# Kernel tuning notes

Hardware: AMD Instinct MI355X
Metric: run time of the kernel (lower is better)

## Reference

```python
import jax, jax.numpy as jnp
import numpy as np

NEG = -1e30


def setup_inputs() -> dict:
    key = jax.random.key(0)
    k1, k2, k3, k4 = jax.random.split(key, 4)
    B, L, T, M = 64, 256, 1600, 80
    probs = jax.random.uniform(k1, (B, L, T), dtype=jnp.float32)
    melspec = jax.random.normal(k2, (B, M, T), dtype=jnp.float32)
    text_lengths = jax.random.randint(k3, (B,), 1, L + 1)   # values in [1, L]
    mel_lengths = jax.random.randint(k4, (B,), 1, T + 1)    # values in [1, T]
    return {"probs": probs, "melspec": melspec,
            "text_lengths": text_lengths, "mel_lengths": mel_lengths}


def reference(probs, melspec, text_lengths, mel_lengths):
    B, L, _ = probs.shape
    T = melspec.shape[2]
    log_prob_matrix = jnp.log(probs + 1e-30)            # [B, L, T]
    lp_t = jnp.moveaxis(log_prob_matrix, 2, 0)          # [T, B, L]

    # t = 0: only (l=0, t=0) is alive
    init = jnp.full((B, L), NEG, dtype=log_prob_matrix.dtype)
    init = init.at[:, 0].set(lp_t[0, :, 0])

    def step(prev, lp):
        # stay at label l, or advance from label l-1 (monotonic alignment)
        shifted = jnp.concatenate(
            [jnp.full((B, 1), NEG, dtype=prev.dtype), prev[:, :-1]], axis=1)
        new = jnp.logaddexp(prev, shifted) + lp
        return new, new

    _, ys = jax.lax.scan(step, init, lp_t[1:])          # ys: [T-1, B, L]
    log_alpha = jnp.concatenate([init[None], ys], axis=0)  # [T, B, L]

    b = jnp.arange(B)
    alpha_last = log_alpha[mel_lengths - 1, b, text_lengths - 1]  # [B]
    mdn_loss = -alpha_last.mean()
    return (mdn_loss, log_prob_matrix)
```

## Files before the change

kernel.cpp:

```cpp
#include <hip/hip_runtime.h>

#define LN2f 0.69314718055994531f

constexpr int T_C  = 1600;
constexpr int L_C  = 256;
constexpr int DP_B = 64;
constexpr int CK   = 32;
constexpr int LOGB = 960;

__device__ __forceinline__ float shift_up1_f(float x, bool f15, bool f31) {
    int xi  = __float_as_int(x);
    int s   = __builtin_amdgcn_update_dpp(0, xi, 0x111, 0xF, 0xF, true);
    int b15 = __builtin_amdgcn_update_dpp(0, xi, 0x142, 0xF, 0xF, true);
    int b31 = __builtin_amdgcn_update_dpp(0, xi, 0x143, 0xF, 0xF, true);
    int r = f15 ? b15 : s;
    r     = f31 ? b31 : r;
    return __int_as_float(r);
}
__device__ __forceinline__ int shift_up1_i(int x, bool f15, bool f31) {
    int s   = __builtin_amdgcn_update_dpp(0, x, 0x111, 0xF, 0xF, true);
    int b15 = __builtin_amdgcn_update_dpp(0, x, 0x142, 0xF, 0xF, true);
    int b31 = __builtin_amdgcn_update_dpp(0, x, 0x143, 0xF, 0xF, true);
    int r = f15 ? b15 : s;
    r     = f31 ? b31 : r;
    return r;
}

__global__ __launch_bounds__(256, 1) void fused_kernel(
    const float* __restrict__ probs,
    const int* __restrict__ text_len,
    const int* __restrict__ mel_len,
    float* __restrict__ out1,
    float* __restrict__ alpha_out,
    int n4)
{
    __shared__ float lds[2][CK][L_C];
    const int b   = blockIdx.x;
    const int tid = threadIdx.x;

    if (b >= DP_B) {
        const int W = LOGB * 256;
        int i = (b - DP_B) * 256 + tid;
        if (i >= n4) return;
        const float4* p4 = (const float4*)probs;
        float4 v = p4[i];
        for (;;) {
            const int  nx   = i + W;
            const bool more = nx < n4;
            float4 vn;
            if (more) vn = p4[nx];
            const int o = 4 * i;
            out1[o + 0] = __logf(v.x + 1e-30f);
            out1[o + 1] = __logf(v.y + 1e-30f);
            out1[o + 2] = __logf(v.z + 1e-30f);
            out1[o + 3] = __logf(v.w + 1e-30f);
            if (!more) return;
            v = vn; i = nx;
        }
    }

    const int wv   = tid >> 6;
    const int lane = tid & 63;
    const int ml1  = mel_len[b] - 1;
    const int trip = (ml1 >> 5) + 1;

    if (wv != 0) {
        asm volatile("s_setprio 1");
        const int  pw   = wv - 1;
        const int  f0   = pw * 64 + lane;
        const int  q    = f0 & 7;
        const int  row0 = f0 >> 3;
        const bool lok  = pw < 2;
        const float* gbase = probs + (size_t)b * (L_C * T_C)
                           + (size_t)row0 * T_C + q * 4;
        const int swz0 = 8 * (q & 3);
        const int a0q  = q * 1024;

        float4 rA[11], rB[11];
        auto LD = [&](float4 (&r)[11], int ck) {
            const float* p = gbase + ck * CK;
#pragma unroll
            for (int it = 0; it < 11; ++it)
                if (it < 10 || lok)
                    r[it] = *(const float4*)(p + it * (24 * T_C));
        };
        auto WR = [&](float4 (&r)[11], int bb) {
            float* Lw = &lds[bb][0][0];
#pragma unroll
            for (int it = 0; it < 11; ++it) {
                if (it < 10 || lok) {
                    const int rw = (row0 + 24 * it) ^ swz0;
                    const int A0 = a0q + rw;
                    Lw[A0]             = r[it].x + 1e-30f;
                    Lw[A0 + 256]       = r[it].y + 1e-30f;
                    Lw[(A0 ^ 4) + 512] = r[it].z + 1e-30f;
                    Lw[(A0 ^ 4) + 768] = r[it].w + 1e-30f;
                }
            }
        };

        LD(rA, 0);
        if (trip > 1) LD(rB, 1);
        WR(rA, 0);
        for (int w = 0; w < trip; ++w) {
            __syncthreads();
            if ((w & 1) == 0) {
                if (w + 2 < trip) LD(rA, w + 2);
                if (w + 1 < trip) WR(rB, 1);
            } else {
                if (w + 2 < trip) LD(rB, w + 2);
                if (w + 1 < trip) WR(rA, 0);
            }
        }
        return;
    }

    asm volatile("s_setprio 3");
    const int  cl  = text_len[b] - 1;
    const bool f15 = (lane == 16) | (lane == 48);
    const bool f31 = (lane == 32);
    const int  xr  = 4 * lane;

    float a0 = 0.f, a1 = 0.f, a2 = 0.f, a3 = 0.f;
    int   E = 0;
    bool  alive = (lane == 0);
    float s0 = 0.f, s1 = 0.f, s2 = 0.f, s3 = 0.f;
    int   sE = 0;

    auto renorm = [&]() {
        float m = fmaxf(fmaxf(a0, a1), fmaxf(a2, a3));
        int e = ((__float_as_int(m) >> 23) & 255) - 127;
        e = (m > 0.0f) ? e : 0;
        a0 = ldexpf(a0, -e); a1 = ldexpf(a1, -e);
        a2 = ldexpf(a2, -e); a3 = ldexpf(a3, -e);
        E += e;
    };

    for (int w = 0; w < trip; ++w) {
        __syncthreads();
        const float* Lr = &lds[w & 1][0][0];
        const int tb = w << 5;

        auto ldc = [&](int j) -> float4 {
            return *(const float4*)(Lr + j * 256 + (xr ^ (4 * ((j >> 1) & 7))));
        };
        auto step_full = [&](int j) {
            const float4 c = ldc(j);
            float top = shift_up1_f(a3, f15, f31);
            int   tE  = shift_up1_i(E, f15, f31);
            float contrib = alive ? ldexpf(top, tE - E) : top;
            E = alive ? E : tE;
            alive = alive | (top != 0.0f);
            float n0 = (a0 + contrib) * c.x;
            float n1 = (a1 + a0) * c.y;
            float n2 = (a2 + a1) * c.z;
            float n3 = (a3 + a2) * c.w;
            a0 = n0; a1 = n1; a2 = n2; a3 = n3;
            if (tb + j == ml1) { s0 = a0; s1 = a1; s2 = a2; s3 = a3; sE = E; }
        };

        if (w == 0) {
            const float4 c = ldc(0);
            a0 = (lane == 0) ? c.x : 0.0f;
            if (ml1 == 0) s0 = a0;
#pragma unroll
            for (int j = 1; j < CK; ++j) {
                step_full(j);
                if ((j & 15) == 15) renorm();
            }
        } else if (w < 8) {
#pragma unroll
            for (int j = 0; j < CK; ++j) {
                step_full(j);
                if ((j & 15) == 15) renorm();
            }
        } else {
#pragma unroll
            for (int h = 0; h < 2; ++h) {
                const int tE = shift_up1_i(E, f15, f31);
                const int dE = tE - E;
#pragma unroll
                for (int jj = 0; jj < 16; ++jj) {
                    const int j = h * 16 + jj;
                    const float4 c = ldc(j);
                    float top = shift_up1_f(a3, f15, f31);
                    float contrib = ldexpf(top, dE);
                    float n0 = (a0 + contrib) * c.x;
                    float n1 = (a1 + a0) * c.y;
                    float n2 = (a2 + a1) * c.z;
                    float n3 = (a3 + a2) * c.w;
                    a0 = n0; a1 = n1; a2 = n2; a3 = n3;
                    if (tb + j == ml1) { s0 = a0; s1 = a1; s2 = a2; s3 = a3; sE = E; }
                }
                renorm();
            }
        }
    }

    if (lane == (cl >> 2)) {
        const int jj = cl & 3;
        float v = (jj == 0) ? s0 : (jj == 1) ? s1 : (jj == 2) ? s2 : s3;
        v = fmaxf(v, 1e-44f);
        const float res = (log2f(v) + (float)sE) * LN2f;
        alpha_out[b] = (cl > ml1) ? -1e30f : res;
    }
}

__global__ void loss_kernel(const float* __restrict__ alpha,
                            float* __restrict__ out, int B) {
    float v = (threadIdx.x < B) ? alpha[threadIdx.x] : 0.0f;
#pragma unroll
    for (int off = 32; off > 0; off >>= 1) v += __shfl_down(v, off, 64);
    if (threadIdx.x == 0) out[0] = -v / (float)B;
}

extern "C" void kernel_launch(void* const* d_in, const int* in_sizes, int n_in,
                              void* d_out, int out_size, void* d_ws, size_t ws_size,
                              hipStream_t stream) {
    const float* probs    = (const float*)d_in[0];
    const int*   text_len = (const int*)d_in[2];
    const int*   mel_len  = (const int*)d_in[3];
    float* out = (float*)d_out;

    const int B  = in_sizes[2];
    const int n  = in_sizes[0];
    const int n4 = n / 4;
    const int G  = DP_B + LOGB;

    fused_kernel<<<G, 256, 0, stream>>>(probs, text_len, mel_len,
                                        out + 1, (float*)d_ws, n4);
    loss_kernel<<<1, 64, 0, stream>>>((const float*)d_ws, out, B);
}
```

Baseline: 264.3 us.

## Halve DP chunk, raise occupancy, align log stores to output with nontemporal writes

The DP chunk shrinks from 32 to 16 timesteps, and the loader waves are remapped so each holds at most 6 float4 registers. Launch bounds move to 5 blocks per CU and the log-grid grows to 1216 blocks, so log blocks can share CUs with DP blocks. The elementwise log path now shifts by 3 floats so its vector stores land on aligned output addresses (out+1 is misaligned), uses nontemporal stores, and prefetches two iterations ahead. The leftover edge elements move into the loss kernel. Halving the chunk doubles the number of barriers in the serial DP loop, which risks making the latency-critical wave slower.

```diff
diff --git a/kernel.cpp b/kernel.cpp
--- a/kernel.cpp
+++ b/kernel.cpp
@@ -5,8 +5,11 @@
 constexpr int T_C  = 1600;
 constexpr int L_C  = 256;
 constexpr int DP_B = 64;
-constexpr int CK   = 32;
-constexpr int LOGB = 960;
+constexpr int CK   = 16;
+constexpr int LOGB = 1216;
+
+typedef float f4u __attribute__((ext_vector_type(4), aligned(4)));
+typedef float f4a __attribute__((ext_vector_type(4)));
 
 __device__ __forceinline__ float shift_up1_f(float x, bool f15, bool f31) {
     int xi  = __float_as_int(x);
@@ -26,7 +29,7 @@
     return r;
 }
 
-__global__ __launch_bounds__(256, 1) void fused_kernel(
+__global__ __launch_bounds__(256, 5) void fused_kernel(
     const float* __restrict__ probs,
     const int* __restrict__ text_len,
     const int* __restrict__ mel_len,
@@ -40,57 +43,61 @@
 
     if (b >= DP_B) {
         const int W = LOGB * 256;
-        int i = (b - DP_B) * 256 + tid;
-        if (i >= n4) return;
-        const float4* p4 = (const float4*)probs;
-        float4 v = p4[i];
+        const int M = n4 - 1;
+        int m = (b - DP_B) * 256 + tid;
+        if (m >= M) return;
+        const float* src = probs + 3;
+        float*       dst = out1 + 3;
+        f4u v0 = *(const f4u*)(src + 4 * (size_t)m);
+        int  m1 = m + W;
+        bool h1 = m1 < M;
+        f4u v1 = v0;
+        if (h1) v1 = *(const f4u*)(src + 4 * (size_t)m1);
         for (;;) {
-            const int  nx   = i + W;
-            const bool more = nx < n4;
-            float4 vn;
-            if (more) vn = p4[nx];
-            const int o = 4 * i;
-            out1[o + 0] = __logf(v.x + 1e-30f);
-            out1[o + 1] = __logf(v.y + 1e-30f);
-            out1[o + 2] = __logf(v.z + 1e-30f);
-            out1[o + 3] = __logf(v.w + 1e-30f);
-            if (!more) return;
-            v = vn; i = nx;
+            const int  m2 = m1 + W;
+            const bool h2 = m2 < M;
+            f4u v2;
+            if (h2) v2 = *(const f4u*)(src + 4 * (size_t)m2);
+            f4a o;
+            o.x = __logf(v0.x + 1e-30f);
+            o.y = __logf(v0.y + 1e-30f);
+            o.z = __logf(v0.z + 1e-30f);
+            o.w = __logf(v0.w + 1e-30f);
+            __builtin_nontemporal_store(o, (f4a*)(dst + 4 * (size_t)m));
+            if (!h1) return;
+            v0 = v1; v1 = v2; m = m1; m1 = m2; h1 = h2;
         }
     }
 
     const int wv   = tid >> 6;
     const int lane = tid & 63;
     const int ml1  = mel_len[b] - 1;
-    const int trip = (ml1 >> 5) + 1;
+    const int trip = (ml1 >> 4) + 1;
 
     if (wv != 0) {
         asm volatile("s_setprio 1");
-        const int  pw   = wv - 1;
-        const int  f0   = pw * 64 + lane;
-        const int  q    = f0 & 7;
-        const int  row0 = f0 >> 3;
-        const bool lok  = pw < 2;
+        const int pw   = wv - 1;
+        const int q    = lane & 3;
+        const int g    = lane >> 2;
+        const int row0 = pw * 16 + g;
+        const int NIT  = (pw == 0) ? 6 : 5;
         const float* gbase = probs + (size_t)b * (L_C * T_C)
                            + (size_t)row0 * T_C + q * 4;
-        const int swz0 = 8 * (q & 3);
-        const int a0q  = q * 1024;
-
-        float4 rA[11], rB[11];
-        auto LD = [&](float4 (&r)[11], int ck) {
+        const int swz = 8 * q;
+
+        float4 rA[6], rB[6];
+        auto LD = [&](float4 (&r)[6], int ck) {
             const float* p = gbase + ck * CK;
 #pragma unroll
-            for (int it = 0; it < 11; ++it)
-                if (it < 10 || lok)
-                    r[it] = *(const float4*)(p + it * (24 * T_C));
-        };
-        auto WR = [&](float4 (&r)[11], int bb) {
+            for (int it = 0; it < 6; ++it)
+                if (it < NIT) r[it] = *(const float4*)(p + it * (48 * T_C));
+        };
+        auto WR = [&](float4 (&r)[6], int bb) {
             float* Lw = &lds[bb][0][0];
 #pragma unroll
-            for (int it = 0; it < 11; ++it) {
-                if (it < 10 || lok) {
-                    const int rw = (row0 + 24 * it) ^ swz0;
-                    const int A0 = a0q + rw;
+            for (int it = 0; it < 6; ++it) {
+                if (it < NIT) {
+                    const int A0 = q * 1024 + ((row0 + 48 * it) ^ swz);
                     Lw[A0]             = r[it].x + 1e-30f;
                     Lw[A0 + 256]       = r[it].y + 1e-30f;
                     Lw[(A0 ^ 4) + 512] = r[it].z + 1e-30f;
@@ -139,7 +146,7 @@
     for (int w = 0; w < trip; ++w) {
         __syncthreads();
         const float* Lr = &lds[w & 1][0][0];
-        const int tb = w << 5;
+        const int tb = w << 4;
 
         auto ldc = [&](int j) -> float4 {
             return *(const float4*)(Lr + j * 256 + (xr ^ (4 * ((j >> 1) & 7))));
@@ -164,24 +171,18 @@
             a0 = (lane == 0) ? c.x : 0.0f;
             if (ml1 == 0) s0 = a0;
 #pragma unroll
-            for (int j = 1; j < CK; ++j) {
-                step_full(j);
-                if ((j & 15) == 15) renorm();
-            }
-        } else if (w < 8) {
-#pragma unroll
-            for (int j = 0; j < CK; ++j) {
-                step_full(j);
-                if ((j & 15) == 15) renorm();
-            }
+            for (int j = 1; j < CK; ++j) step_full(j);
+            renorm();
+        } else if (w < 16) {
+#pragma unroll
+            for (int j = 0; j < CK; ++j) step_full(j);
+            renorm();
         } else {
-#pragma unroll
-            for (int h = 0; h < 2; ++h) {
-                const int tE = shift_up1_i(E, f15, f31);
-                const int dE = tE - E;
-#pragma unroll
-                for (int jj = 0; jj < 16; ++jj) {
-                    const int j = h * 16 + jj;
+            const int tE = shift_up1_i(E, f15, f31);
+            const int dE = tE - E;
+            if (w == trip - 1) {
+#pragma unroll
+                for (int j = 0; j < CK; ++j) {
                     const float4 c = ldc(j);
                     float top = shift_up1_f(a3, f15, f31);
                     float contrib = ldexpf(top, dE);
@@ -192,8 +193,20 @@
                     a0 = n0; a1 = n1; a2 = n2; a3 = n3;
                     if (tb + j == ml1) { s0 = a0; s1 = a1; s2 = a2; s3 = a3; sE = E; }
                 }
-                renorm();
+            } else {
+#pragma unroll
+                for (int j = 0; j < CK; ++j) {
+                    const float4 c = ldc(j);
+                    float top = shift_up1_f(a3, f15, f31);
+                    float contrib = ldexpf(top, dE);
+                    float n0 = (a0 + contrib) * c.x;
+                    float n1 = (a1 + a0) * c.y;
+                    float n2 = (a2 + a1) * c.z;
+                    float n3 = (a3 + a2) * c.w;
+                    a0 = n0; a1 = n1; a2 = n2; a3 = n3;
+                }
             }
+            renorm();
         }
     }
 
@@ -207,11 +220,15 @@
 }
 
 __global__ void loss_kernel(const float* __restrict__ alpha,
-                            float* __restrict__ out, int B) {
-    float v = (threadIdx.x < B) ? alpha[threadIdx.x] : 0.0f;
+                            const float* __restrict__ probs,
+                            float* __restrict__ out, int B, int n) {
+    const int t = threadIdx.x;
+    if (t < 3)  out[1 + t] = __logf(probs[t] + 1e-30f);
+    if (t == 3) out[n] = __logf(probs[n - 1] + 1e-30f);
+    float v = (t < B) ? alpha[t] : 0.0f;
 #pragma unroll
     for (int off = 32; off > 0; off >>= 1) v += __shfl_down(v, off, 64);
-    if (threadIdx.x == 0) out[0] = -v / (float)B;
+    if (t == 0) out[0] = -v / (float)B;
 }
 
 extern "C" void kernel_launch(void* const* d_in, const int* in_sizes, int n_in,
@@ -229,5 +246,5 @@
 
     fused_kernel<<<G, 256, 0, stream>>>(probs, text_len, mel_len,
                                         out + 1, (float*)d_ws, n4);
-    loss_kernel<<<1, 64, 0, stream>>>((const float*)d_ws, out, B);
-}
+    loss_kernel<<<1, 64, 0, stream>>>((const float*)d_ws, probs, out, B, n);
+}
```

Result: slower. 270.2 us (+2.2%).
